# Optimization experiments

Hardware: AMD Instinct MI355X
Metric: run time of the kernel (lower is better)

The kernel has to match this reference:

```python
import jax, jax.numpy as jnp
import numpy as np

N, E, F, H, HEADS, L, G = 16384, 262144, 16, 128, 4, 5, 128
DFF = 4 * H
EPS = 1e-5

def _bn(h, g, b):
    m = h.mean(axis=0)
    v = h.var(axis=0)
    return g * (h - m) / jnp.sqrt(v + EPS) + b

def setup_inputs():
    key = jax.random.key(0)
    ks = jax.random.split(key, 20)
    rn = lambda k, s, fan: jax.random.normal(k, s, jnp.float32) / np.float32(np.sqrt(fan))
    return {
        'x': jax.random.normal(ks[0], (N, F), jnp.float32),
        'edge_index': jax.random.randint(ks[1], (2, E), 0, N),
        'batch_index': jnp.sort(jax.random.randint(ks[2], (N,), 0, G)),
        'embW': rn(ks[3], (F, H), F), 'embb': jnp.zeros((H,), jnp.float32),
        'emb_g': jnp.ones((H,), jnp.float32), 'emb_be': jnp.zeros((H,), jnp.float32),
        'Wq': rn(ks[4], (L, H, HEADS * H), H), 'bq': jnp.zeros((L, HEADS * H), jnp.float32),
        'Wk': rn(ks[5], (L, H, HEADS * H), H), 'bk': jnp.zeros((L, HEADS * H), jnp.float32),
        'Wv': rn(ks[6], (L, H, HEADS * H), H), 'bv': jnp.zeros((L, HEADS * H), jnp.float32),
        'Wskip': rn(ks[7], (L, H, H), H), 'bskip': jnp.zeros((L, H), jnp.float32),
        'Wbeta': rn(ks[8], (L, 3 * H, 1), 3 * H),
        'W1': rn(ks[9], (L, H, DFF), H), 'b1': jnp.zeros((L, DFF), jnp.float32),
        'g1': jnp.ones((L, DFF), jnp.float32), 'be1': jnp.zeros((L, DFF), jnp.float32),
        'W2': rn(ks[10], (L, DFF, H), DFF), 'b2': jnp.zeros((L, H), jnp.float32),
        'predW': rn(ks[11], (H, 1), H), 'predb': jnp.zeros((1,), jnp.float32),
    }

def reference(x, edge_index, batch_index, embW, embb, emb_g, emb_be, Wq, bq, Wk, bk, Wv, bv, Wskip, bskip, Wbeta, W1, b1, g1, be1, W2, b2, predW, predb):
    src, dst = edge_index[0], edge_index[1]
    h = jax.nn.gelu(_bn(x @ embW + embb, emb_g, emb_be), approximate=False)
    scale = jnp.float32(1.0 / np.sqrt(H))  # sqrt(out_channels) per PyG TransformerConv

    def layer(h, p):
        Wq_, bq_, Wk_, bk_, Wv_, bv_, Ws_, bs_, Wb_, W1_, b1_, g1_, be1_, W2_, b2_ = p
        q = (h @ Wq_ + bq_).reshape(N, HEADS, H)
        k = (h @ Wk_ + bk_).reshape(N, HEADS, H)
        v = (h @ Wv_ + bv_).reshape(N, HEADS, H)
        logits = jnp.einsum('ehc,ehc->eh', q[dst], k[src]) * scale  # [E, HEADS]
        m = jax.ops.segment_max(logits, dst, num_segments=N)
        p_e = jnp.exp(logits - m[dst])
        denom = jax.ops.segment_sum(p_e, dst, num_segments=N) + 1e-16
        agg = jax.ops.segment_sum(p_e[:, :, None] * v[src], dst, num_segments=N)
        out = (agg / denom[:, :, None]).mean(axis=1)  # concat=False -> mean over heads
        x_r = h @ Ws_ + bs_
        beta = jax.nn.sigmoid(jnp.concatenate([out, x_r, out - x_r], axis=-1) @ Wb_)  # [N,1]
        out = beta * x_r + (1.0 - beta) * out
        hh = jax.nn.gelu(_bn(out @ W1_ + b1_, g1_, be1_), approximate=False)
        return hh @ W2_ + b2_

    def step(carry, p):
        return layer(carry, p), None

    h, _ = jax.lax.scan(step, h, (Wq, bq, Wk, bk, Wv, bv, Wskip, bskip, Wbeta, W1, b1, g1, be1, W2, b2))
    pooled = jax.ops.segment_max(h, batch_index, num_segments=G)  # MaxAggregation
    return (pooled @ predW + predb).reshape(-1)
```

## Files before the change

### kernel.cpp

```cpp
#include <hip/hip_runtime.h>
#include <hip/hip_bf16.h>

using bf16 = __hip_bfloat16;
typedef __attribute__((ext_vector_type(8))) short bf16x8;
typedef __attribute__((ext_vector_type(4))) float f32x4;

constexpr int N_   = 16384;
constexpr int E_   = 262144;
constexpr int F_   = 16;
constexpr int H_   = 128;
constexpr int NF1_ = 640;
constexpr int DFF_ = 512;
constexpr int G_   = 128;
constexpr int L_   = 5;
constexpr float EPS_ = 1e-5f;

constexpr int WCAT1SZ = NF1_ * 128;
constexpr int W1TSZ   = 512 * 128;
constexpr int W2TSZ   = 512 * 128;
constexpr int WVSSZ   = 128 * 512;
constexpr int TRBLKS  = 5 * 144;

__device__ __forceinline__ float gelu_f(float x) {
  return 0.5f * x * (1.0f + erff(x * 0.70710678118654752440f));
}

__device__ __forceinline__ void unpack8(const uint4 w, float* f) {
  f[0] = __uint_as_float(w.x << 16); f[1] = __uint_as_float(w.x & 0xFFFF0000u);
  f[2] = __uint_as_float(w.y << 16); f[3] = __uint_as_float(w.y & 0xFFFF0000u);
  f[4] = __uint_as_float(w.z << 16); f[5] = __uint_as_float(w.z & 0xFFFF0000u);
  f[6] = __uint_as_float(w.w << 16); f[7] = __uint_as_float(w.w & 0xFFFF0000u);
}

__global__ __launch_bounds__(256) void k_ptrans(
    const float* __restrict__ Ws, const float* __restrict__ W1,
    const float* __restrict__ W2, const float* __restrict__ bs,
    const float* __restrict__ bv,
    bf16* __restrict__ Wcat1, bf16* __restrict__ W1t, bf16* __restrict__ W2t,
    float* __restrict__ bcat, float* __restrict__ bvm) {
  __shared__ float lds[32][33];
  const int b = blockIdx.x;
  if (b >= TRBLKS) {
    int j = (b - TRBLKS) * 256 + threadIdx.x;
    if (j < 5 * NF1_) {
      int l = j / NF1_, c = j % NF1_;
      if (c >= 512) bcat[j] = bs[l * 128 + (c - 512)];
    } else if (j < 5 * NF1_ + 5 * 128) {
      int j2 = j - 5 * NF1_;
      int l = j2 / 128, n = j2 % 128;
      bvm[j2] = 0.25f * (bv[l * 512 + n] + bv[l * 512 + 128 + n]
                       + bv[l * 512 + 256 + n] + bv[l * 512 + 384 + n]);
    }
    return;
  }
  const int l = b / 144, t = b % 144;
  const float* src; int C; bf16* dst; int dld; int nof; int tt;
  if (t < 16) {
    tt = t;
    src = Ws + (size_t)l * 128 * 128; C = 128;
    dst = Wcat1 + (size_t)l * WCAT1SZ; dld = 128; nof = 512;
  } else if (t < 80) {
    tt = t - 16;
    src = W1 + (size_t)l * 128 * 512; C = 512;
    dst = W1t + (size_t)l * W1TSZ; dld = 128; nof = 0;
  } else {
    tt = t - 80;
    src = W2 + (size_t)l * 512 * 128; C = 128;
    dst = W2t + (size_t)l * W2TSZ; dld = 512; nof = 0;
  }
  const int tpr = C >> 5;
  const int r0 = (tt / tpr) * 32, c0 = (tt % tpr) * 32;
  const int j = threadIdx.x & 31, g = threadIdx.x >> 5;
#pragma unroll
  for (int ii = 0; ii < 4; ++ii) {
    int i = g * 4 + ii;
    lds[i][j] = src[(size_t)(r0 + i) * C + c0 + j];
  }
  __syncthreads();
#pragma unroll
  for (int ii = 0; ii < 4; ++ii) {
    int i = g * 4 + ii;
    dst[(size_t)(nof + c0 + i) * dld + r0 + j] = __float2bfloat16(lds[j][i]);
  }
}

__global__ __launch_bounds__(256) void k_wvprep(const float* __restrict__ Wv,
                                                bf16* __restrict__ Wvs) {
  __shared__ float lds[32][33];
  const int b = blockIdx.x;
  const int l = b / 64, rest = b % 64;
  const int h = rest / 16, tt = rest % 16;
  const int r0 = (tt / 4) * 32, c0 = (tt % 4) * 32;
  const float* src = Wv + (size_t)l * 128 * 512 + h * 128;
  bf16* dst = Wvs + (size_t)l * WVSSZ;
  const int j = threadIdx.x & 31, g = threadIdx.x >> 5;
#pragma unroll
  for (int ii = 0; ii < 4; ++ii) {
    int i = g * 4 + ii;
    lds[i][j] = src[(size_t)(r0 + i) * 512 + c0 + j];
  }
  __syncthreads();
#pragma unroll
  for (int ii = 0; ii < 4; ++ii) {
    int i = g * 4 + ii;
    dst[(size_t)(c0 + i) * 512 + h * 128 + r0 + j] = __float2bfloat16(0.25f * lds[j][i]);
  }
}

__global__ __launch_bounds__(256) void k_gmat(
    const float* __restrict__ Wq, const float* __restrict__ Wk,
    const float* __restrict__ bq,
    bf16* __restrict__ Wcat1, float* __restrict__ bcat) {
  __shared__ float lq[32][132];
  __shared__ float lk[32][132];
  const int l = blockIdx.x >> 2, h = blockIdx.x & 3;
  const int half = blockIdx.y;
  const int tid = threadIdx.x;
  const int c = tid & 127, ch = tid >> 7;
  const int cp0 = half * 64 + ch * 32;
  const float* wqL = Wq + (size_t)l * 128 * 512 + h * 128;
  const float* wkL = Wk + (size_t)l * 128 * 512 + h * 128;
  float acc[32];
#pragma unroll
  for (int j = 0; j < 32; ++j) acc[j] = 0.f;
  for (int a0 = 0; a0 < 128; a0 += 32) {
    __syncthreads();
#pragma unroll
    for (int q4 = 0; q4 < 4; ++q4) {
      int f4 = tid * 4 + q4;
      int row = f4 >> 3, af = f4 & 7;
      float4 gq = *reinterpret_cast<const float4*>(wqL + (size_t)row * 512 + a0 + af * 4);
      float4 gk = *reinterpret_cast<const float4*>(wkL + (size_t)row * 512 + a0 + af * 4);
      lq[af * 4 + 0][row] = gq.x; lq[af * 4 + 1][row] = gq.y;
      lq[af * 4 + 2][row] = gq.z; lq[af * 4 + 3][row] = gq.w;
      lk[af * 4 + 0][row] = gk.x; lk[af * 4 + 1][row] = gk.y;
      lk[af * 4 + 2][row] = gk.z; lk[af * 4 + 3][row] = gk.w;
    }
    __syncthreads();
    for (int a = 0; a < 32; ++a) {
      float wq = lq[a][c];
#pragma unroll
      for (int j = 0; j < 32; ++j) acc[j] = fmaf(wq, lk[a][cp0 + j], acc[j]);
    }
  }
  bf16* gt = Wcat1 + (size_t)l * WCAT1SZ;
#pragma unroll
  for (int j = 0; j < 32; ++j)
    gt[(size_t)(h * 128 + cp0 + j) * 128 + c] = __float2bfloat16(acc[j]);
  if (half == 0 && ch == 0) {
    float s = 0.f;
    const float* wkr = wkL + (size_t)c * 512;
    const float* bqh = bq + (size_t)l * 512 + h * 128;
    for (int a = 0; a < 128; ++a) s = fmaf(wkr[a], bqh[a], s);
    bcat[(size_t)l * NF1_ + h * 128 + c] = s;
  }
}

__global__ __launch_bounds__(256) void k_embed2(const float* __restrict__ x,
    const float* __restrict__ W, const float* __restrict__ b,
    float* __restrict__ out, float* __restrict__ ss, float* __restrict__ sq) {
  __shared__ float xs[128][16];
  __shared__ float wsm[16][128];
  __shared__ float sr[2][128], qr[2][128];
  const int blk = blockIdx.x;
  const int t = threadIdx.x;
  for (int i = t; i < 16 * 128; i += 256) wsm[i >> 7][i & 127] = W[i];
  for (int i = t; i < 128 * 16; i += 256) xs[i >> 4][i & 15] = x[(size_t)blk * 2048 + i];
  __syncthreads();
  const int c = t & 127, rg = t >> 7;
  float bc = b[c];
  float s = 0.f, q = 0.f;
  for (int r = rg * 64; r < rg * 64 + 64; ++r) {
    float v = bc;
#pragma unroll
    for (int f = 0; f < 16; ++f) v = fmaf(xs[r][f], wsm[f][c], v);
    out[(size_t)(blk * 128 + r) * 128 + c] = v;
    s += v; q += v * v;
  }
  sr[rg][c] = s; qr[rg][c] = q;
  __syncthreads();
  if (t < 128) { ss[blk * 128 + t] = sr[0][t] + sr[1][t]; sq[blk * 128 + t] = qr[0][t] + qr[1][t]; }
}

template<int NC>
__global__ void k_bn_finalize(const float* __restrict__ sums, const float* __restrict__ sumsq,
                              const float* __restrict__ g, const float* __restrict__ be,
                              float* __restrict__ a, float* __restrict__ cc) {
  int c = blockIdx.x * 128 + threadIdx.x;
  if (c >= NC) return;
  float s = 0.f, q = 0.f;
  for (int b = 0; b < 128; ++b) { s += sums[b * NC + c]; q += sumsq[b * NC + c]; }
  float mean = s * (1.0f / N_);
  float var  = q * (1.0f / N_) - mean * mean;
  float inv  = rsqrtf(var + EPS_);
  float aa   = g[c] * inv;
  a[c]  = aa;
  cc[c] = be[c] - aa * mean;
}

template<int NC>
__global__ void k_bn_apply_gelu_cast(const float* __restrict__ xin, const float* __restrict__ a,
                                     const float* __restrict__ cc, bf16* __restrict__ outb) {
  int i4 = (blockIdx.x * 256 + threadIdx.x) * 4;
  int c = i4 & (NC - 1);
  float4 v = *reinterpret_cast<const float4*>(xin + i4);
  union { uint2 u2; bf16 h[4]; } pk;
  pk.h[0] = __float2bfloat16(gelu_f(fmaf(a[c + 0], v.x, cc[c + 0])));
  pk.h[1] = __float2bfloat16(gelu_f(fmaf(a[c + 1], v.y, cc[c + 1])));
  pk.h[2] = __float2bfloat16(gelu_f(fmaf(a[c + 2], v.z, cc[c + 2])));
  pk.h[3] = __float2bfloat16(gelu_f(fmaf(a[c + 3], v.w, cc[c + 3])));
  *reinterpret_cast<uint2*>(outb + i4) = pk.u2;
}

__global__ void k_count(const int* __restrict__ dst, int* __restrict__ deg) {
  int e = blockIdx.x * 256 + threadIdx.x;
  if (e < E_) atomicAdd(&deg[dst[e]], 1);
}

__global__ void k_bsum(const int* __restrict__ deg, int* __restrict__ bsum) {
  __shared__ int sh[256];
  int t = threadIdx.x;
  sh[t] = deg[blockIdx.x * 256 + t];
  __syncthreads();
  for (int d = 128; d > 0; d >>= 1) { if (t < d) sh[t] += sh[t + d]; __syncthreads(); }
  if (t == 0) bsum[blockIdx.x] = sh[0];
}

__global__ void k_boffs(const int* __restrict__ deg, const int* __restrict__ bsum,
                        int* __restrict__ offs) {
  __shared__ int sh[256];
  __shared__ int baseSh;
  int t = threadIdx.x;
  if (t < 64) {
    int v = bsum[t];
    int s = v;
    for (int d = 1; d < 64; d <<= 1) { int o = __shfl_up(s, d); if (t >= d) s += o; }
    if (t == (int)blockIdx.x) baseSh = s - v;
  }
  int v = deg[blockIdx.x * 256 + t];
  sh[t] = v;
  __syncthreads();
  for (int d = 1; d < 256; d <<= 1) {
    int add = (t >= d) ? sh[t - d] : 0;
    __syncthreads();
    sh[t] += add;
    __syncthreads();
  }
  offs[blockIdx.x * 256 + t] = baseSh + sh[t] - v;
  if (blockIdx.x == 63 && t == 255) offs[N_] = E_;
}

__global__ void k_scatter(const int* __restrict__ src, const int* __restrict__ dst,
                          const int* __restrict__ off, int* __restrict__ cursor,
                          int* __restrict__ srcs) {
  int e = blockIdx.x * 256 + threadIdx.x;
  if (e < E_) {
    int d = dst[e];
    int pos = off[d] + atomicAdd(&cursor[d], 1);
    srcs[pos] = src[e];
  }
}

template<int KDIM, int NOUT, int TM, int MODE>
__global__ __launch_bounds__(256) void k_mfma(
    const bf16* __restrict__ A, const float* __restrict__ Af,
    const bf16* __restrict__ BT, const float* __restrict__ bias,
    float* __restrict__ outF, bf16* __restrict__ outB,
    float* __restrict__ zfp, float* __restrict__ xrp,
    float* __restrict__ ss, float* __restrict__ sq,
    const float* __restrict__ aCol, const float* __restrict__ cCol) {
  constexpr int MF = TM / 32;
  __shared__ bf16 As[TM][72];
  __shared__ bf16 Bs[128][72];
  __shared__ float sred[2][128], qred[2][128];
  __shared__ float aS[MODE == 4 ? KDIM : 1], cS[MODE == 4 ? KDIM : 1];
  const int tid = threadIdx.x;
  const int wid = tid >> 6, lane = tid & 63;
  const int wr = wid >> 1, wc = wid & 1;
  const int m0 = blockIdx.x * TM, n0 = blockIdx.y * 128;
  const int ln = lane & 15, lq = lane >> 4;
  if constexpr (MODE == 4) {
    for (int i = tid; i < KDIM; i += 256) { aS[i] = aCol[i]; cS[i] = cCol[i]; }
    __syncthreads();
  }
  f32x4 acc[MF][4];
#pragma unroll
  for (int i = 0; i < MF; ++i)
#pragma unroll
    for (int j = 0; j < 4; ++j) acc[i][j] = (f32x4){0.f, 0.f, 0.f, 0.f};

  for (int k0 = 0; k0 < KDIM; k0 += 64) {
#pragma unroll
    for (int u = tid; u < TM * 8; u += 256) {
      int r = u >> 3, c = u & 7;
      if constexpr (MODE == 4) {
        const float4* ap = reinterpret_cast<const float4*>(Af + (size_t)(m0 + r) * KDIM + k0 + c * 8);
        float4 f0 = ap[0], f1 = ap[1];
        float f[8] = {f0.x, f0.y, f0.z, f0.w, f1.x, f1.y, f1.z, f1.w};
        int colb = k0 + c * 8;
        union { uint4 u4; bf16 h[8]; } pk;
#pragma unroll
        for (int j = 0; j < 8; ++j)
          pk.h[j] = __float2bfloat16(gelu_f(fmaf(aS[colb + j], f[j], cS[colb + j])));
        *(uint4*)(&As[r][c * 8]) = pk.u4;
      } else {
        *(uint4*)(&As[r][c * 8]) = *(const uint4*)(A + (size_t)(m0 + r) * KDIM + k0 + c * 8);
      }
    }
#pragma unroll
    for (int u = tid; u < 1024; u += 256) {
      int r = u >> 3, c = u & 7;
      *(uint4*)(&Bs[r][c * 8]) = *(const uint4*)(BT + (size_t)(n0 + r) * KDIM + k0 + c * 8);
    }
    __syncthreads();
#pragma unroll
    for (int kk = 0; kk < 2; ++kk) {
      bf16x8 af[MF], bg[4];
#pragma unroll
      for (int i = 0; i < MF; ++i)
        af[i] = *(const bf16x8*)(&As[wr * (TM / 2) + i * 16 + ln][kk * 32 + lq * 8]);
#pragma unroll
      for (int j = 0; j < 4; ++j)
        bg[j] = *(const bf16x8*)(&Bs[wc * 64 + j * 16 + ln][kk * 32 + lq * 8]);
#pragma unroll
      for (int i = 0; i < MF; ++i)
#pragma unroll
        for (int j = 0; j < 4; ++j)
          acc[i][j] = __builtin_amdgcn_mfma_f32_16x16x32_bf16(af[i], bg[j], acc[i][j], 0, 0, 0);
    }
    __syncthreads();
  }
  float ssj[4] = {0.f, 0.f, 0.f, 0.f}, sqj[4] = {0.f, 0.f, 0.f, 0.f};
#pragma unroll
  for (int i = 0; i < MF; ++i) {
#pragma unroll
    for (int j = 0; j < 4; ++j) {
      int gcol = n0 + wc * 64 + j * 16 + ln;
      float bv = 0.f;
      if constexpr (MODE != 5) bv = bias[gcol];
      int row0 = m0 + wr * (TM / 2) + i * 16 + lq * 4;
#pragma unroll
      for (int qq = 0; qq < 4; ++qq) {
        float val = acc[i][j][qq] + bv;
        int row = row0 + qq;
        if (MODE == 3) {
          outF[(size_t)row * NOUT + gcol] = val;
          ssj[j] += val; sqj[j] += val * val;
        } else if (MODE == 4) {
          outF[(size_t)row * NOUT + gcol] = val;
          outB[(size_t)row * NOUT + gcol] = __float2bfloat16(val);
        } else if (MODE == 5) {
          outF[(size_t)row * NOUT + gcol] = val;
        } else {
          if (n0 < 512) zfp[(size_t)row * 512 + gcol] = val;
          else          xrp[(size_t)row * H_ + (gcol - 512)] = val;
        }
      }
    }
  }
  if constexpr (MODE == 3) {
#pragma unroll
    for (int j = 0; j < 4; ++j) {
      ssj[j] += __shfl_xor(ssj[j], 16); ssj[j] += __shfl_xor(ssj[j], 32);
      sqj[j] += __shfl_xor(sqj[j], 16); sqj[j] += __shfl_xor(sqj[j], 32);
    }
    if (lq == 0) {
#pragma unroll
      for (int j = 0; j < 4; ++j) {
        sred[wr][wc * 64 + j * 16 + ln] = ssj[j];
        qred[wr][wc * 64 + j * 16 + ln] = sqj[j];
      }
    }
    __syncthreads();
    if (tid < 128) {
      ss[(size_t)blockIdx.x * NOUT + n0 + tid] = sred[0][tid] + sred[1][tid];
      sq[(size_t)blockIdx.x * NOUT + n0 + tid] = qred[0][tid] + qred[1][tid];
    }
  }
}

__global__ __launch_bounds__(256) void k_attn(const float* __restrict__ zf,
    const bf16* __restrict__ hb, const int* __restrict__ srcs,
    const int* __restrict__ off, bf16* __restrict__ aggB) {
  const int wave = threadIdx.x >> 6;
  const int lane = threadIdx.x & 63;
  const int bid = blockIdx.x;
  const int swz = ((bid & 7) << 9) | (bid >> 3);
  const int node = swz * 4 + wave;
  const int sub = lane & 15;
  const float scale = 0.08838834764831845f;
  float qf[8];
  {
    const float4* qp = reinterpret_cast<const float4*>(zf + (size_t)node * 512) + lane * 2;
    float4 a = qp[0], b = qp[1];
    qf[0]=a.x; qf[1]=a.y; qf[2]=a.z; qf[3]=a.w;
    qf[4]=b.x; qf[5]=b.y; qf[6]=b.z; qf[7]=b.w;
  }
  float m = -1e30f, den = 0.f;
  float acc[8] = {0.f, 0.f, 0.f, 0.f, 0.f, 0.f, 0.f, 0.f};
  const int s0 = off[node], s1 = off[node + 1];
  if (s0 < s1) {
    int i0 = srcs[s0];
    int i1 = (s0 + 1 < s1) ? srcs[s0 + 1] : i0;
    uint4 h0 = *(const uint4*)(hb + (size_t)i0 * 128 + sub * 8);
    uint4 h1 = *(const uint4*)(hb + (size_t)i1 * 128 + sub * 8);
    for (int t = s0; t < s1; t += 2) {
      int j0 = (t + 2 < s1) ? srcs[t + 2] : i0;
      int j1 = (t + 3 < s1) ? srcs[t + 3] : i0;
      uint4 nh0 = *(const uint4*)(hb + (size_t)j0 * 128 + sub * 8);
      uint4 nh1 = *(const uint4*)(hb + (size_t)j1 * 128 + sub * 8);
      {
        float hf[8]; unpack8(h0, hf);
        float p = hf[0]*qf[0]+hf[1]*qf[1]+hf[2]*qf[2]+hf[3]*qf[3]
                + hf[4]*qf[4]+hf[5]*qf[5]+hf[6]*qf[6]+hf[7]*qf[7];
        p += __shfl_xor(p, 1); p += __shfl_xor(p, 2);
        p += __shfl_xor(p, 4); p += __shfl_xor(p, 8);
        float logit = p * scale;
        if (logit > m + 8.f) {
          float co = __expf(m - logit);
          den *= co;
#pragma unroll
          for (int j = 0; j < 8; ++j) acc[j] *= co;
          m = logit;
        }
        float pe = __expf(logit - m);
        den += pe;
#pragma unroll
        for (int j = 0; j < 8; ++j) acc[j] = fmaf(pe, hf[j], acc[j]);
      }
      if (t + 1 < s1) {
        float hf[8]; unpack8(h1, hf);
        float p = hf[0]*qf[0]+hf[1]*qf[1]+hf[2]*qf[2]+hf[3]*qf[3]
                + hf[4]*qf[4]+hf[5]*qf[5]+hf[6]*qf[6]+hf[7]*qf[7];
        p += __shfl_xor(p, 1); p += __shfl_xor(p, 2);
        p += __shfl_xor(p, 4); p += __shfl_xor(p, 8);
        float logit = p * scale;
        if (logit > m + 8.f) {
          float co = __expf(m - logit);
          den *= co;
#pragma unroll
          for (int j = 0; j < 8; ++j) acc[j] *= co;
          m = logit;
        }
        float pe = __expf(logit - m);
        den += pe;
#pragma unroll
        for (int j = 0; j < 8; ++j) acc[j] = fmaf(pe, hf[j], acc[j]);
      }
      h0 = nh0; h1 = nh1;
    }
  }
  float inv = 1.f / (den + 1e-16f);
  union { uint4 u4; bf16 h[8]; } pk;
#pragma unroll
  for (int j = 0; j < 8; ++j) pk.h[j] = __float2bfloat16(acc[j] * inv);
  *reinterpret_cast<uint4*>(aggB + (size_t)node * 512 + lane * 8) = pk.u4;
}

__global__ __launch_bounds__(256) void k_beta(const float* __restrict__ out0,
    const float* __restrict__ xr, const float* __restrict__ Wb,
    const float* __restrict__ bvm, const int* __restrict__ off,
    bf16* __restrict__ gated) {
  const int wave = threadIdx.x >> 6;
  const int lane = threadIdx.x & 63;
  const int node = blockIdx.x * 4 + wave;
  const int c0 = lane * 2;
  bool hasE = off[node + 1] > off[node];
  float2 o = *reinterpret_cast<const float2*>(out0 + (size_t)node * H_ + c0);
  if (hasE) { o.x += bvm[c0]; o.y += bvm[c0 + 1]; }
  float2 xv = *reinterpret_cast<const float2*>(xr + (size_t)node * H_ + c0);
  float s = o.x * (Wb[c0] + Wb[256 + c0]) + xv.x * (Wb[128 + c0] - Wb[256 + c0])
          + o.y * (Wb[c0 + 1] + Wb[256 + c0 + 1]) + xv.y * (Wb[128 + c0 + 1] - Wb[256 + c0 + 1]);
#pragma unroll
  for (int d = 1; d < 64; d <<= 1) s += __shfl_xor(s, d);
  float beta = 1.f / (1.f + __expf(-s));
  union { unsigned u; bf16 h[2]; } pk;
  pk.h[0] = __float2bfloat16(beta * xv.x + (1.f - beta) * o.x);
  pk.h[1] = __float2bfloat16(beta * xv.y + (1.f - beta) * o.y);
  *reinterpret_cast<unsigned*>(gated + (size_t)node * H_ + c0) = pk.u;
}

__global__ __launch_bounds__(256) void k_poolpred(const float* __restrict__ h,
    const int* __restrict__ batch, const float* __restrict__ predW,
    const float* __restrict__ predb, float* __restrict__ out) {
  __shared__ float cm[2][128];
  __shared__ int range[2];
  const int g = blockIdx.x, t = threadIdx.x;
  if (t < 2) {
    int target = g + t;
    int lo = 0, hi = N_;
    while (lo < hi) { int mid = (lo + hi) >> 1; if (batch[mid] < target) lo = mid + 1; else hi = mid; }
    range[t] = lo;
  }
  __syncthreads();
  const int lo = range[0], hi = range[1];
  const int c = t & 127, rg = t >> 7;
  float m = -3.402823466e+38f;
  for (int r = lo + rg; r < hi; r += 2) m = fmaxf(m, h[(size_t)r * H_ + c]);
  cm[rg][c] = m;
  __syncthreads();
  if (t < 64) {
    float m0 = fmaxf(cm[0][t], cm[1][t]);
    float m1 = fmaxf(cm[0][t + 64], cm[1][t + 64]);
    float s = m0 * predW[t] + m1 * predW[t + 64];
#pragma unroll
    for (int d = 1; d < 64; d <<= 1) s += __shfl_xor(s, d);
    if (t == 0) out[g] = s + predb[0];
  }
}

extern "C" void kernel_launch(void* const* d_in, const int* in_sizes, int n_in,
                              void* d_out, int out_size, void* d_ws, size_t ws_size,
                              hipStream_t stream) {
  const float* x      = (const float*)d_in[0];
  const int*   edge   = (const int*)d_in[1];
  const int*   esrc   = edge;
  const int*   edst   = edge + E_;
  const int*   batch  = (const int*)d_in[2];
  const float* embW   = (const float*)d_in[3];
  const float* embb   = (const float*)d_in[4];
  const float* emb_g  = (const float*)d_in[5];
  const float* emb_be = (const float*)d_in[6];
  const float* Wq     = (const float*)d_in[7];
  const float* bq     = (const float*)d_in[8];
  const float* Wk     = (const float*)d_in[9];
  const float* Wv     = (const float*)d_in[11];
  const float* bv     = (const float*)d_in[12];
  const float* Wskip  = (const float*)d_in[13];
  const float* bskip  = (const float*)d_in[14];
  const float* Wbeta  = (const float*)d_in[15];
  const float* W1     = (const float*)d_in[16];
  const float* b1     = (const float*)d_in[17];
  const float* g1     = (const float*)d_in[18];
  const float* be1    = (const float*)d_in[19];
  const float* W2     = (const float*)d_in[20];
  const float* b2     = (const float*)d_in[21];
  const float* predW  = (const float*)d_in[22];
  const float* predb  = (const float*)d_in[23];

  float* ws = (float*)d_ws;
  size_t o = 0;
  auto alloc_f = [&](size_t n) { float* p = ws + o; o += n; return p; };
  float* A32   = alloc_f((size_t)N_ * 512);
  float* B32   = alloc_f((size_t)N_ * H_);
  float* xr    = alloc_f((size_t)N_ * H_);
  float* stats = alloc_f(2 * 128 * DFF_);
  float* a_c   = alloc_f(DFF_);
  float* c_c   = alloc_f(DFF_);
  float* bcat  = alloc_f(5 * NF1_);
  float* bvm   = alloc_f(5 * 128);
  bf16* bp = (bf16*)(ws + o);
  size_t ob = 0;
  auto alloc_b = [&](size_t n) { bf16* p = bp + ob; ob += n; return p; };
  bf16* aggB = alloc_b((size_t)N_ * 512);
  bf16* hb   = alloc_b((size_t)N_ * H_);
  bf16* gated= alloc_b((size_t)N_ * H_);
  bf16* Wcat1= alloc_b((size_t)5 * WCAT1SZ);
  bf16* W1t  = alloc_b((size_t)5 * W1TSZ);
  bf16* W2t  = alloc_b((size_t)5 * W2TSZ);
  bf16* Wvs  = alloc_b((size_t)5 * WVSSZ);
  int* deg    = (int*)(bp + ob);
  int* offs   = deg + N_;
  int* cursor = offs + N_ + 1;
  int* srcs   = cursor + N_;
  int* bsum   = srcs + E_;

  float* zf   = A32;  float* t1 = A32;
  float* out0 = B32;  float* h32 = B32;

  k_ptrans<<<TRBLKS + 15, 256, 0, stream>>>(Wskip, W1, W2, bskip, bv,
                                            Wcat1, W1t, W2t, bcat, bvm);
  k_wvprep<<<320, 256, 0, stream>>>(Wv, Wvs);
  k_gmat<<<dim3(20, 2), 256, 0, stream>>>(Wq, Wk, bq, Wcat1, bcat);

  hipMemsetAsync(deg, 0, N_ * sizeof(int), stream);
  hipMemsetAsync(cursor, 0, N_ * sizeof(int), stream);
  k_count  <<<E_ / 256, 256, 0, stream>>>(edst, deg);
  k_bsum   <<<64, 256, 0, stream>>>(deg, bsum);
  k_boffs  <<<64, 256, 0, stream>>>(deg, bsum, offs);
  k_scatter<<<E_ / 256, 256, 0, stream>>>(esrc, edst, offs, cursor, srcs);

  k_embed2<<<128, 256, 0, stream>>>(x, embW, embb, A32, stats, stats + 128 * 128);
  k_bn_finalize<128><<<1, 128, 0, stream>>>(stats, stats + 128 * 128, emb_g, emb_be, a_c, c_c);
  k_bn_apply_gelu_cast<128><<<N_ * H_ / 1024, 256, 0, stream>>>(A32, a_c, c_c, hb);

  for (int l = 0; l < L_; ++l) {
    const float* Wb_ = Wbeta + (size_t)l * 3 * H_;
    const float* b1_ = b1 + (size_t)l * DFF_;
    const float* g1_ = g1 + (size_t)l * DFF_;
    const float* be1_= be1 + (size_t)l * DFF_;
    const float* b2_ = b2 + (size_t)l * H_;

    k_mfma<128, NF1_, 128, 2><<<dim3(N_ / 128, NF1_ / 128), 256, 0, stream>>>(
        hb, nullptr, Wcat1 + (size_t)l * WCAT1SZ, bcat + (size_t)l * NF1_,
        nullptr, nullptr, zf, xr, nullptr, nullptr, nullptr, nullptr);

    k_attn<<<N_ / 4, 256, 0, stream>>>(zf, hb, srcs, offs, aggB);

    k_mfma<512, 128, 64, 5><<<dim3(N_ / 64, 1), 256, 0, stream>>>(
        aggB, nullptr, Wvs + (size_t)l * WVSSZ, nullptr,
        out0, nullptr, nullptr, nullptr, nullptr, nullptr, nullptr, nullptr);

    k_beta<<<N_ / 4, 256, 0, stream>>>(out0, xr, Wb_, bvm + (size_t)l * 128, offs, gated);

    k_mfma<128, 512, 128, 3><<<dim3(N_ / 128, 4), 256, 0, stream>>>(
        gated, nullptr, W1t + (size_t)l * W1TSZ, b1_, t1, nullptr, nullptr, nullptr,
        stats, stats + 128 * 512, nullptr, nullptr);

    k_bn_finalize<512><<<4, 128, 0, stream>>>(stats, stats + 128 * 512, g1_, be1_, a_c, c_c);

    k_mfma<512, 128, 64, 4><<<dim3(N_ / 64, 1), 256, 0, stream>>>(
        nullptr, t1, W2t + (size_t)l * W2TSZ, b2_, h32, hb, nullptr, nullptr,
        nullptr, nullptr, a_c, c_c);
  }

  k_poolpred<<<G_, 256, 0, stream>>>(h32, batch, predW, predb, (float*)d_out);
}
```

Before: 765.8 us.

## Add skinny-K GEMM kernel with resident weights; split BN-GELU out of W2 GEMM

```diff
diff --git a/kernel.cpp b/kernel.cpp
--- a/kernel.cpp
+++ b/kernel.cpp
@@ -182,14 +182,14 @@
   if (t < 128) { ss[blk * 128 + t] = sr[0][t] + sr[1][t]; sq[blk * 128 + t] = qr[0][t] + qr[1][t]; }
 }
 
-template<int NC>
+template<int NC, int NP>
 __global__ void k_bn_finalize(const float* __restrict__ sums, const float* __restrict__ sumsq,
                               const float* __restrict__ g, const float* __restrict__ be,
                               float* __restrict__ a, float* __restrict__ cc) {
   int c = blockIdx.x * 128 + threadIdx.x;
   if (c >= NC) return;
   float s = 0.f, q = 0.f;
-  for (int b = 0; b < 128; ++b) { s += sums[b * NC + c]; q += sumsq[b * NC + c]; }
+  for (int b = 0; b < NP; ++b) { s += sums[(size_t)b * NC + c]; q += sumsq[(size_t)b * NC + c]; }
   float mean = s * (1.0f / N_);
   float var  = q * (1.0f / N_) - mean * mean;
   float inv  = rsqrtf(var + EPS_);
@@ -263,26 +263,20 @@
 
 template<int KDIM, int NOUT, int TM, int MODE>
 __global__ __launch_bounds__(256) void k_mfma(
-    const bf16* __restrict__ A, const float* __restrict__ Af,
-    const bf16* __restrict__ BT, const float* __restrict__ bias,
-    float* __restrict__ outF, bf16* __restrict__ outB,
+    const bf16* __restrict__ A, const bf16* __restrict__ BT,
+    const float* __restrict__ bias,
+    float* __restrict__ outF,
     float* __restrict__ zfp, float* __restrict__ xrp,
-    float* __restrict__ ss, float* __restrict__ sq,
-    const float* __restrict__ aCol, const float* __restrict__ cCol) {
+    float* __restrict__ ss, float* __restrict__ sq) {
   constexpr int MF = TM / 32;
   __shared__ bf16 As[TM][72];
   __shared__ bf16 Bs[128][72];
   __shared__ float sred[2][128], qred[2][128];
-  __shared__ float aS[MODE == 4 ? KDIM : 1], cS[MODE == 4 ? KDIM : 1];
   const int tid = threadIdx.x;
   const int wid = tid >> 6, lane = tid & 63;
   const int wr = wid >> 1, wc = wid & 1;
   const int m0 = blockIdx.x * TM, n0 = blockIdx.y * 128;
   const int ln = lane & 15, lq = lane >> 4;
-  if constexpr (MODE == 4) {
-    for (int i = tid; i < KDIM; i += 256) { aS[i] = aCol[i]; cS[i] = cCol[i]; }
-    __syncthreads();
-  }
   f32x4 acc[MF][4];
 #pragma unroll
   for (int i = 0; i < MF; ++i)
@@ -293,19 +287,7 @@
 #pragma unroll
     for (int u = tid; u < TM * 8; u += 256) {
       int r = u >> 3, c = u & 7;
-      if constexpr (MODE == 4) {
-        const float4* ap = reinterpret_cast<const float4*>(Af + (size_t)(m0 + r) * KDIM + k0 + c * 8);
-        float4 f0 = ap[0], f1 = ap[1];
-        float f[8] = {f0.x, f0.y, f0.z, f0.w, f1.x, f1.y, f1.z, f1.w};
-        int colb = k0 + c * 8;
-        union { uint4 u4; bf16 h[8]; } pk;
-#pragma unroll
-        for (int j = 0; j < 8; ++j)
-          pk.h[j] = __float2bfloat16(gelu_f(fmaf(aS[colb + j], f[j], cS[colb + j])));
-        *(uint4*)(&As[r][c * 8]) = pk.u4;
-      } else {
-        *(uint4*)(&As[r][c * 8]) = *(const uint4*)(A + (size_t)(m0 + r) * KDIM + k0 + c * 8);
-      }
+      *(uint4*)(&As[r][c * 8]) = *(const uint4*)(A + (size_t)(m0 + r) * KDIM + k0 + c * 8);
     }
 #pragma unroll
     for (int u = tid; u < 1024; u += 256) {
@@ -336,8 +318,7 @@
 #pragma unroll
     for (int j = 0; j < 4; ++j) {
       int gcol = n0 + wc * 64 + j * 16 + ln;
-      float bv = 0.f;
-      if constexpr (MODE != 5) bv = bias[gcol];
+      float bv = bias[gcol];
       int row0 = m0 + wr * (TM / 2) + i * 16 + lq * 4;
 #pragma unroll
       for (int qq = 0; qq < 4; ++qq) {
@@ -346,14 +327,9 @@
         if (MODE == 3) {
           outF[(size_t)row * NOUT + gcol] = val;
           ssj[j] += val; sqj[j] += val * val;
-        } else if (MODE == 4) {
-          outF[(size_t)row * NOUT + gcol] = val;
-          outB[(size_t)row * NOUT + gcol] = __float2bfloat16(val);
-        } else if (MODE == 5) {
-          outF[(size_t)row * NOUT + gcol] = val;
         } else {
-          if (n0 < 512) zfp[(size_t)row * 512 + gcol] = val;
-          else          xrp[(size_t)row * H_ + (gcol - 512)] = val;
+          if (gcol < 512) zfp[(size_t)row * 512 + gcol] = val;
+          else            xrp[(size_t)row * H_ + (gcol - 512)] = val;
         }
       }
     }
@@ -375,6 +351,62 @@
     if (tid < 128) {
       ss[(size_t)blockIdx.x * NOUT + n0 + tid] = sred[0][tid] + sred[1][tid];
       sq[(size_t)blockIdx.x * NOUT + n0 + tid] = qred[0][tid] + qred[1][tid];
+    }
+  }
+}
+
+template<int KDIM, int NOUT, int CSPL, int MODE>
+__global__ __launch_bounds__(256) void k_sgemm(
+    const bf16* __restrict__ A, const bf16* __restrict__ BT,
+    const float* __restrict__ bias,
+    float* __restrict__ outF, bf16* __restrict__ outB) {
+  constexpr int KS = KDIM / 32;
+  constexpr int NCOL = NOUT / CSPL;
+  constexpr int NFR = NCOL / 16;
+  __shared__ bf16 Bs[NFR][KS][64][8];
+  const int tid = threadIdx.x;
+  const int wid = tid >> 6, lane = tid & 63;
+  const int ln = lane & 15, lq = lane >> 4;
+  const int nc0 = blockIdx.y * NCOL;
+  for (int idx = tid; idx < NCOL * (KDIM / 8); idx += 256) {
+    int col = idx / (KDIM / 8);
+    int oct = idx % (KDIM / 8);
+    uint4 w = *(const uint4*)(BT + (size_t)(nc0 + col) * KDIM + oct * 8);
+    int ks = oct >> 2, q = oct & 3;
+    *(uint4*)(&Bs[col >> 4][ks][q * 16 + (col & 15)][0]) = w;
+  }
+  __syncthreads();
+  const int m0 = blockIdx.x * 64 + wid * 16;
+  bf16x8 a[KS];
+  const bf16* ap = A + (size_t)(m0 + ln) * KDIM + lq * 8;
+#pragma unroll
+  for (int ks = 0; ks < KS; ++ks) a[ks] = *(const bf16x8*)(ap + ks * 32);
+  const int orow = m0 + lq * 4;
+#pragma unroll
+  for (int nf = 0; nf < NFR; ++nf) {
+    f32x4 acc0 = (f32x4){0.f, 0.f, 0.f, 0.f};
+    f32x4 acc1 = (f32x4){0.f, 0.f, 0.f, 0.f};
+#pragma unroll
+    for (int ks = 0; ks < KS; ks += 2) {
+      acc0 = __builtin_amdgcn_mfma_f32_16x16x32_bf16(a[ks],     *(const bf16x8*)(&Bs[nf][ks][lane][0]),     acc0, 0, 0, 0);
+      acc1 = __builtin_amdgcn_mfma_f32_16x16x32_bf16(a[ks + 1], *(const bf16x8*)(&Bs[nf][ks + 1][lane][0]), acc1, 0, 0, 0);
+    }
+    const int col = nc0 + nf * 16 + ln;
+    float bv = 0.f;
+    if constexpr (MODE == 6) bv = bias[col];
+    float v0 = (acc0[0] + acc1[0]) + bv;
+    float v1 = (acc0[1] + acc1[1]) + bv;
+    float v2 = (acc0[2] + acc1[2]) + bv;
+    float v3 = (acc0[3] + acc1[3]) + bv;
+    outF[(size_t)(orow + 0) * NOUT + col] = v0;
+    outF[(size_t)(orow + 1) * NOUT + col] = v1;
+    outF[(size_t)(orow + 2) * NOUT + col] = v2;
+    outF[(size_t)(orow + 3) * NOUT + col] = v3;
+    if constexpr (MODE == 6) {
+      outB[(size_t)(orow + 0) * NOUT + col] = __float2bfloat16(v0);
+      outB[(size_t)(orow + 1) * NOUT + col] = __float2bfloat16(v1);
+      outB[(size_t)(orow + 2) * NOUT + col] = __float2bfloat16(v2);
+      outB[(size_t)(orow + 3) * NOUT + col] = __float2bfloat16(v3);
     }
   }
 }
@@ -466,9 +498,10 @@
   const int node = blockIdx.x * 4 + wave;
   const int c0 = lane * 2;
   bool hasE = off[node + 1] > off[node];
-  float2 o = *reinterpret_cast<const float2*>(out0 + (size_t)node * H_ + c0);
+  const size_t base = (size_t)node * H_ + c0;
+  float2 o = *reinterpret_cast<const float2*>(out0 + base);
   if (hasE) { o.x += bvm[c0]; o.y += bvm[c0 + 1]; }
-  float2 xv = *reinterpret_cast<const float2*>(xr + (size_t)node * H_ + c0);
+  float2 xv = *reinterpret_cast<const float2*>(xr + base);
   float s = o.x * (Wb[c0] + Wb[256 + c0]) + xv.x * (Wb[128 + c0] - Wb[256 + c0])
           + o.y * (Wb[c0 + 1] + Wb[256 + c0 + 1]) + xv.y * (Wb[128 + c0 + 1] - Wb[256 + c0 + 1]);
 #pragma unroll
@@ -477,7 +510,7 @@
   union { unsigned u; bf16 h[2]; } pk;
   pk.h[0] = __float2bfloat16(beta * xv.x + (1.f - beta) * o.x);
   pk.h[1] = __float2bfloat16(beta * xv.y + (1.f - beta) * o.y);
-  *reinterpret_cast<unsigned*>(gated + (size_t)node * H_ + c0) = pk.u;
+  *reinterpret_cast<unsigned*>(gated + base) = pk.u;
 }
 
 __global__ __launch_bounds__(256) void k_poolpred(const float* __restrict__ h,
@@ -544,7 +577,7 @@
   float* A32   = alloc_f((size_t)N_ * 512);
   float* B32   = alloc_f((size_t)N_ * H_);
   float* xr    = alloc_f((size_t)N_ * H_);
-  float* stats = alloc_f(2 * 128 * DFF_);
+  float* stats = alloc_f((size_t)2 * 128 * DFF_);
   float* a_c   = alloc_f(DFF_);
   float* c_c   = alloc_f(DFF_);
   float* bcat  = alloc_f(5 * NF1_);
@@ -567,6 +600,7 @@
 
   float* zf   = A32;  float* t1 = A32;
   float* out0 = B32;  float* h32 = B32;
+  bf16*  t1b  = aggB;
 
   k_ptrans<<<TRBLKS + 15, 256, 0, stream>>>(Wskip, W1, W2, bskip, bv,
                                             Wcat1, W1t, W2t, bcat, bvm);
@@ -581,7 +615,7 @@
   k_scatter<<<E_ / 256, 256, 0, stream>>>(esrc, edst, offs, cursor, srcs);
 
   k_embed2<<<128, 256, 0, stream>>>(x, embW, embb, A32, stats, stats + 128 * 128);
-  k_bn_finalize<128><<<1, 128, 0, stream>>>(stats, stats + 128 * 128, emb_g, emb_be, a_c, c_c);
+  k_bn_finalize<128, 128><<<1, 128, 0, stream>>>(stats, stats + 128 * 128, emb_g, emb_be, a_c, c_c);
   k_bn_apply_gelu_cast<128><<<N_ * H_ / 1024, 256, 0, stream>>>(A32, a_c, c_c, hb);
 
   for (int l = 0; l < L_; ++l) {
@@ -592,26 +626,27 @@
     const float* b2_ = b2 + (size_t)l * H_;
 
     k_mfma<128, NF1_, 128, 2><<<dim3(N_ / 128, NF1_ / 128), 256, 0, stream>>>(
-        hb, nullptr, Wcat1 + (size_t)l * WCAT1SZ, bcat + (size_t)l * NF1_,
-        nullptr, nullptr, zf, xr, nullptr, nullptr, nullptr, nullptr);
+        hb, Wcat1 + (size_t)l * WCAT1SZ, bcat + (size_t)l * NF1_,
+        nullptr, zf, xr, nullptr, nullptr);
 
     k_attn<<<N_ / 4, 256, 0, stream>>>(zf, hb, srcs, offs, aggB);
 
-    k_mfma<512, 128, 64, 5><<<dim3(N_ / 64, 1), 256, 0, stream>>>(
-        aggB, nullptr, Wvs + (size_t)l * WVSSZ, nullptr,
-        out0, nullptr, nullptr, nullptr, nullptr, nullptr, nullptr, nullptr);
+    k_sgemm<512, 128, 2, 5><<<dim3(N_ / 64, 2), 256, 0, stream>>>(
+        aggB, Wvs + (size_t)l * WVSSZ, nullptr, out0, nullptr);
 
     k_beta<<<N_ / 4, 256, 0, stream>>>(out0, xr, Wb_, bvm + (size_t)l * 128, offs, gated);
 
     k_mfma<128, 512, 128, 3><<<dim3(N_ / 128, 4), 256, 0, stream>>>(
-        gated, nullptr, W1t + (size_t)l * W1TSZ, b1_, t1, nullptr, nullptr, nullptr,
-        stats, stats + 128 * 512, nullptr, nullptr);
-
-    k_bn_finalize<512><<<4, 128, 0, stream>>>(stats, stats + 128 * 512, g1_, be1_, a_c, c_c);
-
-    k_mfma<512, 128, 64, 4><<<dim3(N_ / 64, 1), 256, 0, stream>>>(
-        nullptr, t1, W2t + (size_t)l * W2TSZ, b2_, h32, hb, nullptr, nullptr,
-        nullptr, nullptr, a_c, c_c);
+        gated, W1t + (size_t)l * W1TSZ, b1_,
+        t1, nullptr, nullptr, stats, stats + 128 * 512);
+
+    k_bn_finalize<512, 128><<<4, 128, 0, stream>>>(
+        stats, stats + 128 * 512, g1_, be1_, a_c, c_c);
+
+    k_bn_apply_gelu_cast<512><<<N_ * DFF_ / 1024, 256, 0, stream>>>(t1, a_c, c_c, t1b);
+
+    k_sgemm<512, 128, 2, 6><<<dim3(N_ / 64, 2), 256, 0, stream>>>(
+        t1b, W2t + (size_t)l * W2TSZ, b2_, h32, hb);
   }
 
   k_poolpred<<<G_, 256, 0, stream>>>(h32, batch, predW, predb, (float*)d_out);
```

New measurement: 685.5 us (median of 2 runs). 1.12x faster.
